# Optimization experiments

Hardware: AMD Instinct MI355X
Metric: run time of the kernel (lower is better)

## Reference

```python
import jax, jax.numpy as jnp
import numpy as np

# ---- problem sizes ----
N_NEURONS = 1536
N_INPUTS = 768
BATCH = 32
T = 256
DT = 1.0  # ms per step
SURRGRAD_SCALE = 10.0

# ---- per-cell-type physiology (recurrent): 0=excitatory, 1=inhibitory ----
CELL_TAU_MEM = np.array([20.0, 10.0], np.float32)   # ms
CELL_THETA   = np.array([-50.0, -50.0], np.float32) # mV
CELL_URESET  = np.array([-65.0, -65.0], np.float32) # mV
CELL_EL      = np.array([-65.0, -65.0], np.float32) # mV
CELL_GL      = np.array([10.0, 10.0], np.float32)   # nS
CELL_TAUREF  = np.array([2.0, 1.0], np.float32)     # ms

# ---- synapse types: AMPA(pre=exc), NMDA(pre=exc), GABA_A(pre=inh) ----
SYN_CELL_ID   = np.array([0, 0, 1], np.int32)
SYN_TAU_RISE  = np.array([0.5, 2.0, 0.5], np.float32)
SYN_TAU_DECAY = np.array([2.0, 100.0, 5.0], np.float32)
SYN_EREV      = np.array([0.0, 0.0, -70.0], np.float32)
SYN_GBAR      = np.array([1.0, 0.5, 1.0], np.float32)

# ---- feedforward: single excitatory input type, single AMPA synapse ----
FF_TAU_RISE, FF_TAU_DECAY, FF_EREV, FF_GBAR = 0.5, 2.0, 0.0, 1.0


@jax.custom_vjp
def spike(v):
    # Heaviside spike with fast-sigmoid surrogate gradient
    return (v >= 0).astype(v.dtype)

def _spike_fwd(v):
    return spike(v), v

def _spike_bwd(v, g):
    return (g / (SURRGRAD_SCALE * jnp.abs(v) + 1.0) ** 2,)

spike.defvjp(_spike_fwd, _spike_bwd)


def setup_inputs() -> dict:
    key = jax.random.key(0)
    ks = jax.random.split(key, 6)
    input_spikes = (jax.random.uniform(ks[0], (BATCH, T, N_INPUTS)) < 0.05).astype(jnp.float32)
    weights = jax.random.normal(ks[1], (N_NEURONS, N_NEURONS), jnp.float32) * 0.05
    weights_FF = jax.random.normal(ks[2], (N_INPUTS, N_NEURONS), jnp.float32) * 0.05
    cell_type_indices = jax.random.randint(ks[3], (N_NEURONS,), 0, 2, jnp.int32)
    cell_type_indices_FF = jnp.zeros((N_INPUTS,), jnp.int32)
    scaling_factors = jax.random.uniform(ks[4], (2, 2), jnp.float32, 0.5, 1.5)
    scaling_factors_FF = jax.random.uniform(ks[5], (1, 2), jnp.float32, 0.5, 1.5)
    return {
        'input_spikes': input_spikes,
        'weights': weights,
        'weights_FF': weights_FF,
        'scaling_factors': scaling_factors,
        'scaling_factors_FF': scaling_factors_FF,
        'cell_type_indices': cell_type_indices,
        'cell_type_indices_FF': cell_type_indices_FF,
    }


def _simulate(input_spikes, weights, weights_FF, scaling_factors, scaling_factors_FF,
              cell_type_indices, cell_type_indices_FF):
    ct = cell_type_indices
    B = input_spikes.shape[0]

    # per-neuron physiology gathered by cell type
    tau_mem = jnp.asarray(CELL_TAU_MEM)[ct]
    theta = jnp.asarray(CELL_THETA)[ct]
    u_reset = jnp.asarray(CELL_URESET)[ct]
    e_l = jnp.asarray(CELL_EL)[ct]
    g_l = jnp.asarray(CELL_GL)[ct]
    ref_steps = jnp.asarray(CELL_TAUREF)[ct] / DT
    leak_coef = DT / (tau_mem * g_l)  # dt / C_m

    # effective weights: cell-type scaling + presynaptic synapse-type mask
    sf = scaling_factors[ct[:, None], ct[None, :]]            # (N, N)
    W = weights * sf
    pre_mask = (jnp.asarray(SYN_CELL_ID)[:, None] == ct[None, :]).astype(W.dtype)  # (S, N)
    Ws = W[None, :, :] * pre_mask[:, :, None]                  # (S, N, N)
    sfF = scaling_factors_FF[cell_type_indices_FF[:, None], ct[None, :]]
    WF = weights_FF * sfF                                      # (n_in, N)

    alpha_r = jnp.exp(-DT / jnp.asarray(SYN_TAU_RISE))[:, None, None]   # (S,1,1)
    alpha_d = jnp.exp(-DT / jnp.asarray(SYN_TAU_DECAY))[:, None, None]
    arF = jnp.exp(jnp.float32(-DT / FF_TAU_RISE))
    adF = jnp.exp(jnp.float32(-DT / FF_TAU_DECAY))
    gbar = jnp.asarray(SYN_GBAR)
    gbarE = jnp.asarray(SYN_GBAR * SYN_EREV)
    S = gbar.shape[0]

    U0 = jnp.broadcast_to(e_l, (B, N_NEURONS))
    carry0 = (U0,
              jnp.zeros((B, N_NEURONS), jnp.float32),       # previous spikes
              jnp.zeros((S, B, N_NEURONS), jnp.float32),    # x (rise)
              jnp.zeros((S, B, N_NEURONS), jnp.float32),    # g (decay)
              jnp.zeros((B, N_NEURONS), jnp.float32),       # x_FF
              jnp.zeros((B, N_NEURONS), jnp.float32),       # g_FF
              jnp.zeros((B, N_NEURONS), jnp.float32))       # refractory counter

    def step(carry, I_t):
        U, s_prev, x, g, xF, gF, ref = carry
        # dual-exponential conductance update per synapse type
        inp = jnp.einsum('bn,snm->sbm', s_prev, Ws)
        x = alpha_r * x + inp
        g = alpha_d * g + x
        xF = arF * xF + I_t @ WF
        gF = adF * gF + xF
        # conductance-based synaptic current: sum_s gbar_s * g_s * (E_s - U)
        gtot = jnp.einsum('s,sbn->bn', gbar, g) + FF_GBAR * gF
        gE = jnp.einsum('s,sbn->bn', gbarE, g) + (FF_GBAR * FF_EREV) * gF
        I_syn = gE - gtot * U
        # leaky membrane integration
        U_new = U + leak_coef * (g_l * (e_l - U) + I_syn)
        # refractory clamp
        in_ref = ref > 0
        U_new = jnp.where(in_ref, u_reset, U_new)
        ref = jnp.maximum(ref - 1.0, 0.0)
        # surrogate-gradient spike and reset
        s_new = spike(U_new - theta)
        U_out = jnp.where(s_new > 0, u_reset, U_new)
        ref = jnp.where(s_new > 0, ref_steps, ref)
        return (U_out, s_new, x, g, xF, gF, ref), (s_new, U_out)

    I_seq = jnp.transpose(input_spikes, (1, 0, 2))  # (T, B, n_in)
    _, (spk, volts) = jax.lax.scan(step, carry0, I_seq)
    return jnp.transpose(spk, (1, 0, 2)), jnp.transpose(volts, (1, 0, 2))


def reference(input_spikes, weights, weights_FF, scaling_factors, scaling_factors_FF,
              cell_type_indices, cell_type_indices_FF):
    return _simulate(input_spikes, weights, weights_FF, scaling_factors, scaling_factors_FF,
                     cell_type_indices, cell_type_indices_FF)
```

## Files before the change

kernel.cpp:

```cpp
#include <hip/hip_runtime.h>
#include <stdint.h>


__global__ __launch_bounds__(768) void snn_lif_kernel(
    const float* __restrict__ I,
    const float* __restrict__ W,
    const float* __restrict__ WF,
    const float* __restrict__ sf,
    const float* __restrict__ sfF,
    const int*   __restrict__ ct,
    float* __restrict__ out,
    uint64_t* __restrict__ recpub)
{
    const int tid = threadIdx.x;
    const int j   = blockIdx.x & 7;
    const int b   = blockIdx.x >> 3;
    const int wv  = tid >> 6;
    const int wl  = tid & 63;

    __shared__ uint32_t ent[3840];
    __shared__ float    part[3][12][192];
    __shared__ uint32_t totals_sh;
    __shared__ uint32_t ctm32_sh[48];
    __shared__ uint64_t fmask_sh[12];

    for (int r = 0; r < 2; ++r) {
        int c = ct[r * 768 + tid];
        uint64_t bal = __ballot(c != 0);
        if (wl == 0) {
            ctm32_sh[r * 24 + wv * 2]     = (uint32_t)bal;
            ctm32_sh[r * 24 + wv * 2 + 1] = (uint32_t)(bal >> 32);
        }
    }
    __syncthreads();

    const int m = j * 192 + ((tid < 192) ? tid : 0);
    const int   myct = ct[m];
    const float s0m  = sf[myct];
    const float s1m  = sf[2 + myct];
    const float sFm  = sfF[myct];
    const float lc   = (myct == 0) ? (1.0f / 200.0f) : (1.0f / 100.0f);
    const float refsteps = (myct == 0) ? 2.0f : 1.0f;
    const float ar0 = expf(-1.0f / 0.5f),  ad0 = expf(-1.0f / 2.0f);
    const float ar1 = expf(-1.0f / 2.0f),  ad1 = expf(-1.0f / 100.0f);
    const float ar2 = expf(-1.0f / 0.5f),  ad2 = expf(-1.0f / 5.0f);
    const float arF = expf(-1.0f / 0.5f),  adF = expf(-1.0f / 2.0f);

    float U = -65.0f, refc = 0.0f;
    float x0 = 0, g0 = 0, x1 = 0, g1 = 0, x2 = 0, g2 = 0, xF = 0, gF = 0;

    const uint32_t ctw = (wl < 48) ? ctm32_sh[wl] : 0u;
    const int btbase = b * 256;

    for (int t = 0; t < 256; ++t) {
        float iv = __builtin_nontemporal_load(
            &I[(uint32_t)(btbase + t) * 768u + (uint32_t)tid]);
        uint64_t fb = __ballot(iv > 0.5f);
        if (wl == 0) fmask_sh[wv] = fb;
        __syncthreads();

        if (wv == 0) {
            uint32_t sm = 0;
            uint64_t fm = 0;
            uint32_t c0 = 0, c1 = 0, cF = 0;
            if (wl < 48) {
                if (t > 0) {
                    const uint32_t fi = (uint32_t)(btbase + t - 1) * 48u + (uint32_t)wl;
                    uint64_t v;
                    do {
                        v = __hip_atomic_load(&recpub[fi], __ATOMIC_RELAXED,
                                              __HIP_MEMORY_SCOPE_AGENT);
                    } while ((uint32_t)(v >> 32) != (uint32_t)t);
                    sm = (uint32_t)v;
                }
                c0 = __popc(sm & ~ctw);
                c1 = __popc(sm & ctw);
            } else if (wl < 60) {
                fm = fmask_sh[wl - 48];
                cF = __popcll(fm);
            }
            uint32_t pack = c0 | (c1 << 11) | (cF << 22);
            uint32_t incl = pack;
            #pragma unroll
            for (int d = 1; d < 64; d <<= 1) {
                uint32_t u = __shfl_up(incl, d, 64);
                if (wl >= d) incl += u;
            }
            const uint32_t excl = incl - pack;
            if (wl == 59) totals_sh = incl;
            uint32_t p0 = excl & 0x7FFu;
            uint32_t p1 = 1536u + ((excl >> 11) & 0x7FFu);
            uint32_t pF = 3072u + (excl >> 22);
            if (wl < 48) {
                uint32_t mm = sm;
                const uint32_t lanebase = (uint32_t)wl * 32u * 1536u;
                while (mm) {
                    const int bit = __builtin_ctz(mm);
                    mm &= mm - 1;
                    const uint32_t off = lanebase + (uint32_t)bit * 1536u;
                    if ((ctw >> bit) & 1u) ent[p1++] = off;
                    else                   ent[p0++] = off;
                }
            } else if (wl < 60) {
                uint64_t mm = fm;
                const uint32_t lanebase = (uint32_t)(wl - 48) * 64u * 1536u;
                while (mm) {
                    const int bit = __builtin_ctzll(mm);
                    mm &= mm - 1;
                    ent[pF++] = lanebase + (uint32_t)bit * 1536u;
                }
            }
        }
        __syncthreads();

        const uint32_t tp = totals_sh;
        const uint32_t t0 = tp & 0x7FFu;
        const uint32_t t1 = (tp >> 11) & 0x7FFu;
        const uint32_t tF = tp >> 22;
        if (wl < 48) {
            const uint32_t colv = (uint32_t)(j * 48 + wl);
            float4 z0 = make_float4(0.f, 0.f, 0.f, 0.f);
            float4 z1 = z0, zF = z0;
            #pragma unroll 4
            for (uint32_t i = (uint32_t)wv; i < t0; i += 12u) {
                const float4 w = ((const float4*)(W + ent[i]))[colv];
                z0.x += w.x; z0.y += w.y; z0.z += w.z; z0.w += w.w;
            }
            #pragma unroll 4
            for (uint32_t i = (uint32_t)wv; i < t1; i += 12u) {
                const float4 w = ((const float4*)(W + ent[1536u + i]))[colv];
                z1.x += w.x; z1.y += w.y; z1.z += w.z; z1.w += w.w;
            }
            #pragma unroll 4
            for (uint32_t i = (uint32_t)wv; i < tF; i += 12u) {
                const float4 w = ((const float4*)(WF + ent[3072u + i]))[colv];
                zF.x += w.x; zF.y += w.y; zF.z += w.z; zF.w += w.w;
            }
            *(float4*)&part[0][wv][wl * 4] = z0;
            *(float4*)&part[1][wv][wl * 4] = z1;
            *(float4*)&part[2][wv][wl * 4] = zF;
        }
        __syncthreads();

        if (tid < 192) {
            float z0s = 0.f, z1s = 0.f, zFs = 0.f;
            #pragma unroll
            for (int k = 0; k < 12; ++k) {
                z0s += part[0][k][tid];
                z1s += part[1][k][tid];
                zFs += part[2][k][tid];
            }
            z0s *= s0m; z1s *= s1m; zFs *= sFm;
            x0 = ar0 * x0 + z0s;  g0 = ad0 * g0 + x0;
            x1 = ar1 * x1 + z0s;  g1 = ad1 * g1 + x1;
            x2 = ar2 * x2 + z1s;  g2 = ad2 * g2 + x2;
            xF = arF * xF + zFs;  gF = adF * gF + xF;
            const float gtot = g0 + 0.5f * g1 + g2 + gF;
            const float gE   = -70.0f * g2;
            const float Isyn = gE - gtot * U;
            float Un = U + lc * (10.0f * (-65.0f - U) + Isyn);
            if (refc > 0.0f) Un = -65.0f;
            refc = fmaxf(refc - 1.0f, 0.0f);
            const bool s = (Un - (-50.0f)) >= 0.0f;
            const float Uo = s ? -65.0f : Un;
            refc = s ? refsteps : refc;
            U = Uo;
            const uint32_t oidx = (uint32_t)(btbase + t) * 1536u + (uint32_t)m;
            __builtin_nontemporal_store(s ? 1.0f : 0.0f, &out[oidx]);
            __builtin_nontemporal_store(Uo, &out[12582912u + oidx]);
            const uint64_t bal = __ballot(s);
            if (wl == 0 || wl == 32) {
                const uint32_t half = (wl == 0) ? (uint32_t)bal : (uint32_t)(bal >> 32);
                const uint32_t word = (uint32_t)(j * 6 + wv * 2) + (wl == 32 ? 1u : 0u);
                const uint32_t widx = (uint32_t)(btbase + t) * 48u + word;
                const uint64_t v = ((uint64_t)(uint32_t)(t + 1) << 32) | half;
                __hip_atomic_store(&recpub[widx], v, __ATOMIC_RELAXED,
                                   __HIP_MEMORY_SCOPE_AGENT);
            }
        }
    }
}

extern "C" void kernel_launch(void* const* d_in, const int* in_sizes, int n_in,
                              void* d_out, int out_size, void* d_ws, size_t ws_size,
                              hipStream_t stream) {
    const float* I   = (const float*)d_in[0];
    const float* W   = (const float*)d_in[1];
    const float* WF  = (const float*)d_in[2];
    const float* sf  = (const float*)d_in[3];
    const float* sfF = (const float*)d_in[4];
    const int*   ct  = (const int*)d_in[5];

    uint64_t* recpub = (uint64_t*)d_ws;

    snn_lif_kernel<<<dim3(256), dim3(768), 0, stream>>>(
        I, W, WF, sf, sfF, ct, (float*)d_out, recpub);
}
```

Baseline: 874.7 us.

## Overlap feedforward input gather with recurrent spike wait in LIF kernel

Moves the feedforward input compaction one step ahead and computes the feedforward weight sums on waves 1-11 while wave 0 spins on the cross-block recurrent spike flags. Adds a prefetch of the next step's input, s_sleep in the spin loop, larger unroll on the recurrent gathers, and publishes spikes before writing outputs. The aim is to hide feedforward work and input-load latency behind the inter-block synchronisation wait on the critical path. In exchange it uses extra shared memory and more complex ordering of the shared ent/fmask buffers across iterations.

Result: faster. 845.3 us (-3.4%).

```diff
diff --git a/kernel.cpp b/kernel.cpp
--- a/kernel.cpp
+++ b/kernel.cpp
@@ -19,8 +19,11 @@
     const int wl  = tid & 63;
 
     __shared__ uint32_t ent[3840];
-    __shared__ float    part[3][12][192];
+    __shared__ float    partF[11][192];
+    __shared__ float    part0[12][192];
+    __shared__ float    part1[12][192];
     __shared__ uint32_t totals_sh;
+    __shared__ uint32_t tF_sh;
     __shared__ uint32_t ctm32_sh[48];
     __shared__ uint64_t fmask_sh[12];
 
@@ -51,35 +54,57 @@
 
     const uint32_t ctw = (wl < 48) ? ctm32_sh[wl] : 0u;
     const int btbase = b * 256;
+    const uint32_t colv = (uint32_t)(j * 48 + wl);
+
+    {
+        float iv0 = __builtin_nontemporal_load(&I[(uint32_t)btbase * 768u + (uint32_t)tid]);
+        uint64_t fb = __ballot(iv0 > 0.5f);
+        if (wl == 0) fmask_sh[wv] = fb;
+    }
+    __syncthreads();
+    if (wv == 0) {
+        uint64_t fm = 0; uint32_t cF = 0;
+        if (wl < 12) { fm = fmask_sh[wl]; cF = __popcll(fm); }
+        uint32_t incl = cF;
+        #pragma unroll
+        for (int d = 1; d < 64; d <<= 1) {
+            uint32_t u = __shfl_up(incl, d, 64);
+            if (wl >= d) incl += u;
+        }
+        if (wl == 11) tF_sh = incl;
+        if (wl < 12) {
+            uint32_t pF = 3072u + (incl - cF);
+            const uint32_t lanebase = (uint32_t)wl * 64u * 1536u;
+            while (fm) {
+                const int bit = __builtin_ctzll(fm);
+                fm &= fm - 1;
+                ent[pF++] = lanebase + (uint32_t)bit * 1536u;
+            }
+        }
+    }
 
     for (int t = 0; t < 256; ++t) {
-        float iv = __builtin_nontemporal_load(
-            &I[(uint32_t)(btbase + t) * 768u + (uint32_t)tid]);
-        uint64_t fb = __ballot(iv > 0.5f);
-        if (wl == 0) fmask_sh[wv] = fb;
         __syncthreads();
+
+        float iv_next = 0.0f;
+        if (t < 255)
+            iv_next = __builtin_nontemporal_load(
+                &I[(uint32_t)(btbase + t + 1) * 768u + (uint32_t)tid]);
 
         if (wv == 0) {
             uint32_t sm = 0;
-            uint64_t fm = 0;
-            uint32_t c0 = 0, c1 = 0, cF = 0;
-            if (wl < 48) {
-                if (t > 0) {
-                    const uint32_t fi = (uint32_t)(btbase + t - 1) * 48u + (uint32_t)wl;
-                    uint64_t v;
-                    do {
-                        v = __hip_atomic_load(&recpub[fi], __ATOMIC_RELAXED,
-                                              __HIP_MEMORY_SCOPE_AGENT);
-                    } while ((uint32_t)(v >> 32) != (uint32_t)t);
-                    sm = (uint32_t)v;
+            if (wl < 48 && t > 0) {
+                const uint32_t fi = (uint32_t)(btbase + t - 1) * 48u + (uint32_t)wl;
+                for (;;) {
+                    uint64_t v = __hip_atomic_load(&recpub[fi], __ATOMIC_RELAXED,
+                                                   __HIP_MEMORY_SCOPE_AGENT);
+                    if ((uint32_t)(v >> 32) == (uint32_t)t) { sm = (uint32_t)v; break; }
+                    __builtin_amdgcn_s_sleep(1);
                 }
-                c0 = __popc(sm & ~ctw);
-                c1 = __popc(sm & ctw);
-            } else if (wl < 60) {
-                fm = fmask_sh[wl - 48];
-                cF = __popcll(fm);
-            }
-            uint32_t pack = c0 | (c1 << 11) | (cF << 22);
+            }
+            const uint32_t c0 = __popc(sm & ~ctw);
+            const uint32_t c1 = __popc(sm & ctw);
+            uint32_t pack = c0 | (c1 << 16);
             uint32_t incl = pack;
             #pragma unroll
             for (int d = 1; d < 64; d <<= 1) {
@@ -87,11 +112,10 @@
                 if (wl >= d) incl += u;
             }
             const uint32_t excl = incl - pack;
-            if (wl == 59) totals_sh = incl;
-            uint32_t p0 = excl & 0x7FFu;
-            uint32_t p1 = 1536u + ((excl >> 11) & 0x7FFu);
-            uint32_t pF = 3072u + (excl >> 22);
+            if (wl == 47) totals_sh = incl;
             if (wl < 48) {
+                uint32_t p0 = excl & 0xFFFFu;
+                uint32_t p1 = 1536u + (excl >> 16);
                 uint32_t mm = sm;
                 const uint32_t lanebase = (uint32_t)wl * 32u * 1536u;
                 while (mm) {
@@ -101,55 +125,50 @@
                     if ((ctw >> bit) & 1u) ent[p1++] = off;
                     else                   ent[p0++] = off;
                 }
-            } else if (wl < 60) {
-                uint64_t mm = fm;
-                const uint32_t lanebase = (uint32_t)(wl - 48) * 64u * 1536u;
-                while (mm) {
-                    const int bit = __builtin_ctzll(mm);
-                    mm &= mm - 1;
-                    ent[pF++] = lanebase + (uint32_t)bit * 1536u;
-                }
-            }
+            }
+        } else if (wl < 48) {
+            const uint32_t tF = tF_sh;
+            float4 zF = make_float4(0.f, 0.f, 0.f, 0.f);
+            #pragma unroll 4
+            for (uint32_t i = (uint32_t)(wv - 1); i < tF; i += 11u) {
+                const float4 w = ((const float4*)(WF + ent[3072u + i]))[colv];
+                zF.x += w.x; zF.y += w.y; zF.z += w.z; zF.w += w.w;
+            }
+            *(float4*)&partF[wv - 1][wl * 4] = zF;
         }
         __syncthreads();
 
         const uint32_t tp = totals_sh;
-        const uint32_t t0 = tp & 0x7FFu;
-        const uint32_t t1 = (tp >> 11) & 0x7FFu;
-        const uint32_t tF = tp >> 22;
+        const uint32_t t0 = tp & 0xFFFFu;
+        const uint32_t t1 = tp >> 16;
         if (wl < 48) {
-            const uint32_t colv = (uint32_t)(j * 48 + wl);
             float4 z0 = make_float4(0.f, 0.f, 0.f, 0.f);
-            float4 z1 = z0, zF = z0;
-            #pragma unroll 4
+            float4 z1 = z0;
+            #pragma unroll 8
             for (uint32_t i = (uint32_t)wv; i < t0; i += 12u) {
                 const float4 w = ((const float4*)(W + ent[i]))[colv];
                 z0.x += w.x; z0.y += w.y; z0.z += w.z; z0.w += w.w;
             }
-            #pragma unroll 4
+            #pragma unroll 8
             for (uint32_t i = (uint32_t)wv; i < t1; i += 12u) {
                 const float4 w = ((const float4*)(W + ent[1536u + i]))[colv];
                 z1.x += w.x; z1.y += w.y; z1.z += w.z; z1.w += w.w;
             }
-            #pragma unroll 4
-            for (uint32_t i = (uint32_t)wv; i < tF; i += 12u) {
-                const float4 w = ((const float4*)(WF + ent[3072u + i]))[colv];
-                zF.x += w.x; zF.y += w.y; zF.z += w.z; zF.w += w.w;
-            }
-            *(float4*)&part[0][wv][wl * 4] = z0;
-            *(float4*)&part[1][wv][wl * 4] = z1;
-            *(float4*)&part[2][wv][wl * 4] = zF;
+            *(float4*)&part0[wv][wl * 4] = z0;
+            *(float4*)&part1[wv][wl * 4] = z1;
+        }
+        {
+            uint64_t fb = __ballot(iv_next > 0.5f);
+            if (wl == 0) fmask_sh[wv] = fb;
         }
         __syncthreads();
 
         if (tid < 192) {
             float z0s = 0.f, z1s = 0.f, zFs = 0.f;
             #pragma unroll
-            for (int k = 0; k < 12; ++k) {
-                z0s += part[0][k][tid];
-                z1s += part[1][k][tid];
-                zFs += part[2][k][tid];
-            }
+            for (int k = 0; k < 11; ++k) zFs += partF[k][tid];
+            #pragma unroll
+            for (int k = 0; k < 12; ++k) { z0s += part0[k][tid]; z1s += part1[k][tid]; }
             z0s *= s0m; z1s *= s1m; zFs *= sFm;
             x0 = ar0 * x0 + z0s;  g0 = ad0 * g0 + x0;
             x1 = ar1 * x1 + z0s;  g1 = ad1 * g1 + x1;
@@ -162,12 +181,6 @@
             if (refc > 0.0f) Un = -65.0f;
             refc = fmaxf(refc - 1.0f, 0.0f);
             const bool s = (Un - (-50.0f)) >= 0.0f;
-            const float Uo = s ? -65.0f : Un;
-            refc = s ? refsteps : refc;
-            U = Uo;
-            const uint32_t oidx = (uint32_t)(btbase + t) * 1536u + (uint32_t)m;
-            __builtin_nontemporal_store(s ? 1.0f : 0.0f, &out[oidx]);
-            __builtin_nontemporal_store(Uo, &out[12582912u + oidx]);
             const uint64_t bal = __ballot(s);
             if (wl == 0 || wl == 32) {
                 const uint32_t half = (wl == 0) ? (uint32_t)bal : (uint32_t)(bal >> 32);
@@ -176,6 +189,32 @@
                 const uint64_t v = ((uint64_t)(uint32_t)(t + 1) << 32) | half;
                 __hip_atomic_store(&recpub[widx], v, __ATOMIC_RELAXED,
                                    __HIP_MEMORY_SCOPE_AGENT);
+            }
+            const float Uo = s ? -65.0f : Un;
+            refc = s ? refsteps : refc;
+            U = Uo;
+            const uint32_t oidx = (uint32_t)(btbase + t) * 1536u + (uint32_t)m;
+            __builtin_nontemporal_store(s ? 1.0f : 0.0f, &out[oidx]);
+            __builtin_nontemporal_store(Uo, &out[12582912u + oidx]);
+        }
+        if (wv == 0 && t < 255) {
+            uint64_t fm = 0; uint32_t cF = 0;
+            if (wl < 12) { fm = fmask_sh[wl]; cF = __popcll(fm); }
+            uint32_t incl = cF;
+            #pragma unroll
+            for (int d = 1; d < 64; d <<= 1) {
+                uint32_t u = __shfl_up(incl, d, 64);
+                if (wl >= d) incl += u;
+            }
+            if (wl == 11) tF_sh = incl;
+            if (wl < 12) {
+                uint32_t pF = 3072u + (incl - cF);
+                const uint32_t lanebase = (uint32_t)wl * 64u * 1536u;
+                while (fm) {
+                    const int bit = __builtin_ctzll(fm);
+                    fm &= fm - 1;
+                    ent[pF++] = lanebase + (uint32_t)bit * 1536u;
+                }
             }
         }
     }
```

## Decentralize spike-list gathering per wave and double-buffer partial sums

Applied to the files above, without the earlier changes.

Removes the wave-0 prefix-scan and shared entry-list build. Each wave now polls its own four recurrent spike words and directly accumulates the matching weight rows, and it walks its own feedforward ballot mask. The partial-sum buffers are double-buffered so two of the three block barriers per step can be dropped. The next step's input load is prefetched, and the spike publish is moved ahead of the output stores to shorten the cross-block critical path. The trade-off is worse load balance across waves, since each wave's work now depends on how many spikes fall in its own words and rows.

Measured after the change: 750.9 us. -14.2%, faster.

```diff
diff --git a/kernel.cpp b/kernel.cpp
--- a/kernel.cpp
+++ b/kernel.cpp
@@ -18,11 +18,10 @@
     const int wv  = tid >> 6;
     const int wl  = tid & 63;
 
-    __shared__ uint32_t ent[3840];
-    __shared__ float    part[3][12][192];
-    __shared__ uint32_t totals_sh;
+    __shared__ float4   part0[2][12][48];
+    __shared__ float4   part1[2][12][48];
+    __shared__ float4   partF[2][12][48];
     __shared__ uint32_t ctm32_sh[48];
-    __shared__ uint64_t fmask_sh[12];
 
     for (int r = 0; r < 2; ++r) {
         int c = ct[r * 768 + tid];
@@ -49,106 +48,94 @@
     float U = -65.0f, refc = 0.0f;
     float x0 = 0, g0 = 0, x1 = 0, g1 = 0, x2 = 0, g2 = 0, xF = 0, gF = 0;
 
-    const uint32_t ctw = (wl < 48) ? ctm32_sh[wl] : 0u;
-    const int btbase = b * 256;
+    const int  btbase  = b * 256;
+    const bool gl      = (wl < 48);
+    const uint32_t colbase = (uint32_t)(j * 192 + wl * 4);
+
+    uint64_t fmask;
+    {
+        float iv = __builtin_nontemporal_load(
+            &I[(uint32_t)btbase * 768u + (uint32_t)tid]);
+        fmask = __ballot(iv > 0.5f);
+    }
 
     for (int t = 0; t < 256; ++t) {
-        float iv = __builtin_nontemporal_load(
-            &I[(uint32_t)(btbase + t) * 768u + (uint32_t)tid]);
-        uint64_t fb = __ballot(iv > 0.5f);
-        if (wl == 0) fmask_sh[wv] = fb;
-        __syncthreads();
+        float ivn = 0.0f;
+        if (t < 255)
+            ivn = __builtin_nontemporal_load(
+                &I[(uint32_t)(btbase + t + 1) * 768u + (uint32_t)tid]);
 
-        if (wv == 0) {
-            uint32_t sm = 0;
-            uint64_t fm = 0;
-            uint32_t c0 = 0, c1 = 0, cF = 0;
-            if (wl < 48) {
-                if (t > 0) {
-                    const uint32_t fi = (uint32_t)(btbase + t - 1) * 48u + (uint32_t)wl;
-                    uint64_t v;
-                    do {
-                        v = __hip_atomic_load(&recpub[fi], __ATOMIC_RELAXED,
-                                              __HIP_MEMORY_SCOPE_AGENT);
-                    } while ((uint32_t)(v >> 32) != (uint32_t)t);
-                    sm = (uint32_t)v;
-                }
-                c0 = __popc(sm & ~ctw);
-                c1 = __popc(sm & ctw);
-            } else if (wl < 60) {
-                fm = fmask_sh[wl - 48];
-                cF = __popcll(fm);
-            }
-            uint32_t pack = c0 | (c1 << 11) | (cF << 22);
-            uint32_t incl = pack;
-            #pragma unroll
-            for (int d = 1; d < 64; d <<= 1) {
-                uint32_t u = __shfl_up(incl, d, 64);
-                if (wl >= d) incl += u;
-            }
-            const uint32_t excl = incl - pack;
-            if (wl == 59) totals_sh = incl;
-            uint32_t p0 = excl & 0x7FFu;
-            uint32_t p1 = 1536u + ((excl >> 11) & 0x7FFu);
-            uint32_t pF = 3072u + (excl >> 22);
-            if (wl < 48) {
-                uint32_t mm = sm;
-                const uint32_t lanebase = (uint32_t)wl * 32u * 1536u;
-                while (mm) {
-                    const int bit = __builtin_ctz(mm);
-                    mm &= mm - 1;
-                    const uint32_t off = lanebase + (uint32_t)bit * 1536u;
-                    if ((ctw >> bit) & 1u) ent[p1++] = off;
-                    else                   ent[p0++] = off;
-                }
-            } else if (wl < 60) {
-                uint64_t mm = fm;
-                const uint32_t lanebase = (uint32_t)(wl - 48) * 64u * 1536u;
-                while (mm) {
-                    const int bit = __builtin_ctzll(mm);
-                    mm &= mm - 1;
-                    ent[pF++] = lanebase + (uint32_t)bit * 1536u;
+        float4 a0 = make_float4(0.f, 0.f, 0.f, 0.f);
+        float4 a1 = a0, aF = a0;
+
+        {
+            uint64_t mm = fmask;
+            while (mm) {
+                const int bit = __builtin_ctzll(mm);
+                mm &= mm - 1;
+                const uint32_t row = (uint32_t)(wv * 64 + bit);
+                if (gl) {
+                    const float4 w = *(const float4*)(WF + row * 1536u + colbase);
+                    aF.x += w.x; aF.y += w.y; aF.z += w.z; aF.w += w.w;
                 }
             }
         }
-        __syncthreads();
 
-        const uint32_t tp = totals_sh;
-        const uint32_t t0 = tp & 0x7FFu;
-        const uint32_t t1 = (tp >> 11) & 0x7FFu;
-        const uint32_t tF = tp >> 22;
-        if (wl < 48) {
-            const uint32_t colv = (uint32_t)(j * 48 + wl);
-            float4 z0 = make_float4(0.f, 0.f, 0.f, 0.f);
-            float4 z1 = z0, zF = z0;
-            #pragma unroll 4
-            for (uint32_t i = (uint32_t)wv; i < t0; i += 12u) {
-                const float4 w = ((const float4*)(W + ent[i]))[colv];
-                z0.x += w.x; z0.y += w.y; z0.z += w.z; z0.w += w.w;
-            }
-            #pragma unroll 4
-            for (uint32_t i = (uint32_t)wv; i < t1; i += 12u) {
-                const float4 w = ((const float4*)(W + ent[1536u + i]))[colv];
-                z1.x += w.x; z1.y += w.y; z1.z += w.z; z1.w += w.w;
-            }
-            #pragma unroll 4
-            for (uint32_t i = (uint32_t)wv; i < tF; i += 12u) {
-                const float4 w = ((const float4*)(WF + ent[3072u + i]))[colv];
-                zF.x += w.x; zF.y += w.y; zF.z += w.z; zF.w += w.w;
-            }
-            *(float4*)&part[0][wv][wl * 4] = z0;
-            *(float4*)&part[1][wv][wl * 4] = z1;
-            *(float4*)&part[2][wv][wl * 4] = zF;
+        if (t > 0) {
+            uint32_t ready = 0;
+            const uint32_t pbase = (uint32_t)(btbase + t - 1) * 48u + (uint32_t)(wv * 4);
+            do {
+                uint64_t pv = 0;
+                if (wl < 4)
+                    pv = __hip_atomic_load(&recpub[pbase + (uint32_t)wl],
+                                           __ATOMIC_RELAXED, __HIP_MEMORY_SCOPE_AGENT);
+                const uint32_t plo = (uint32_t)pv;
+                const uint32_t phi = (uint32_t)(pv >> 32);
+                #pragma unroll
+                for (int k = 0; k < 4; ++k) {
+                    if (ready & (1u << k)) continue;
+                    const uint32_t tg = __builtin_amdgcn_readlane(phi, k);
+                    if (tg != (uint32_t)t) continue;
+                    ready |= 1u << k;
+                    uint32_t bits = __builtin_amdgcn_readlane(plo, k);
+                    const uint32_t word = (uint32_t)(wv * 4 + k);
+                    const uint32_t cm = ctm32_sh[word];
+                    while (bits) {
+                        const int bit = __builtin_ctz(bits);
+                        bits &= bits - 1;
+                        const uint32_t row = word * 32u + (uint32_t)bit;
+                        if (gl) {
+                            const float4 w = *(const float4*)(W + row * 1536u + colbase);
+                            if ((cm >> bit) & 1u) {
+                                a1.x += w.x; a1.y += w.y; a1.z += w.z; a1.w += w.w;
+                            } else {
+                                a0.x += w.x; a0.y += w.y; a0.z += w.z; a0.w += w.w;
+                            }
+                        }
+                    }
+                }
+            } while (ready != 0xFu);
         }
+
+        const int buf = t & 1;
+        if (gl) {
+            part0[buf][wv][wl] = a0;
+            part1[buf][wv][wl] = a1;
+            partF[buf][wv][wl] = aF;
+        }
+        fmask = __ballot(ivn > 0.5f);
         __syncthreads();
 
         if (tid < 192) {
+            const float* p0 = (const float*)&part0[buf][0][0];
+            const float* p1 = (const float*)&part1[buf][0][0];
+            const float* pF = (const float*)&partF[buf][0][0];
             float z0s = 0.f, z1s = 0.f, zFs = 0.f;
             #pragma unroll
             for (int k = 0; k < 12; ++k) {
-                z0s += part[0][k][tid];
-                z1s += part[1][k][tid];
-                zFs += part[2][k][tid];
+                z0s += p0[k * 192 + tid];
+                z1s += p1[k * 192 + tid];
+                zFs += pF[k * 192 + tid];
             }
             z0s *= s0m; z1s *= s1m; zFs *= sFm;
             x0 = ar0 * x0 + z0s;  g0 = ad0 * g0 + x0;
@@ -162,12 +149,6 @@
             if (refc > 0.0f) Un = -65.0f;
             refc = fmaxf(refc - 1.0f, 0.0f);
             const bool s = (Un - (-50.0f)) >= 0.0f;
-            const float Uo = s ? -65.0f : Un;
-            refc = s ? refsteps : refc;
-            U = Uo;
-            const uint32_t oidx = (uint32_t)(btbase + t) * 1536u + (uint32_t)m;
-            __builtin_nontemporal_store(s ? 1.0f : 0.0f, &out[oidx]);
-            __builtin_nontemporal_store(Uo, &out[12582912u + oidx]);
             const uint64_t bal = __ballot(s);
             if (wl == 0 || wl == 32) {
                 const uint32_t half = (wl == 0) ? (uint32_t)bal : (uint32_t)(bal >> 32);
@@ -177,6 +158,12 @@
                 __hip_atomic_store(&recpub[widx], v, __ATOMIC_RELAXED,
                                    __HIP_MEMORY_SCOPE_AGENT);
             }
+            const float Uo = s ? -65.0f : Un;
+            refc = s ? refsteps : refc;
+            U = Uo;
+            const uint32_t oidx = (uint32_t)(btbase + t) * 1536u + (uint32_t)m;
+            __builtin_nontemporal_store(s ? 1.0f : 0.0f, &out[oidx]);
+            __builtin_nontemporal_store(Uo, &out[12582912u + oidx]);
         }
     }
 }
```
